# Kernel optimization log

Hardware: AMD Instinct MI355X
Metric: run time of the kernel (lower is better)

Reference implementation:

```python
import jax, jax.numpy as jnp
import numpy as np

INPUT_DIM = 512
OUTPUT_DIM = 512
NUM_BASIS = 16
GRID_MIN, GRID_MAX = -2.0, 2.0
LN_EPS = 1e-5


def rbf_basis(x):
    # x: [batch, input_dim] -> [batch, input_dim, num_basis]
    centers = jnp.linspace(GRID_MIN, GRID_MAX, NUM_BASIS, dtype=x.dtype)  # [K]
    h = (GRID_MAX - GRID_MIN) / (NUM_BASIS - 1)
    z = (x[..., None] - centers) / h
    return jnp.exp(-(z * z))


def setup_inputs() -> dict:
    key = jax.random.key(0)
    k1, k2, k3 = jax.random.split(key, 3)
    x = jax.random.normal(k1, (4096, INPUT_DIM), dtype=jnp.float32)
    weights = jax.random.normal(k2, (OUTPUT_DIM, INPUT_DIM, NUM_BASIS), dtype=jnp.float32) * 0.1
    base_weights = jax.random.normal(k3, (OUTPUT_DIM, INPUT_DIM), dtype=jnp.float32) * 0.1
    ln_gamma = jnp.ones((OUTPUT_DIM,), dtype=jnp.float32)
    ln_beta = jnp.zeros((OUTPUT_DIM,), dtype=jnp.float32)
    return {"x": x, "weights": weights, "base_weights": base_weights,
            "ln_gamma": ln_gamma, "ln_beta": ln_beta}


def reference(x, weights, base_weights, ln_gamma, ln_beta):
    # per-edge basis expansion: [B, I, K]
    basis = rbf_basis(x)
    # fused contraction replacing the nested python loops:
    # out[b, j] = sum_{i,k} basis[b, i, k] * weights[j, i, k]
    out = jnp.einsum('bik,jik->bj', basis, weights)
    # residual base activation path
    out = out + jax.nn.silu(x) @ base_weights.T
    # layer norm over output_dim
    mean = jnp.mean(out, axis=-1, keepdims=True)
    var = jnp.var(out, axis=-1, keepdims=True)
    out = (out - mean) * jax.lax.rsqrt(var + LN_EPS) * ln_gamma + ln_beta
    return out
```

## Files before the change

kernel.cpp:

```cpp
#include <hip/hip_runtime.h>
#include <hip/hip_bf16.h>


typedef __bf16 bf16x8 __attribute__((ext_vector_type(8)));
typedef __bf16 bf16x4 __attribute__((ext_vector_type(4)));
typedef float  f32x4  __attribute__((ext_vector_type(4)));

#define KT 8704
#define SPLITS 8
#define KS (KT / SPLITS)
#define NT2 (KS / 64)
#define CPE (4096 * 512)
#define ATILE (256 * 64)

__device__ __forceinline__ void gll16(const __bf16* g, __bf16* l) {
    __builtin_amdgcn_global_load_lds(
        (const __attribute__((address_space(1))) void*)g,
        (__attribute__((address_space(3))) void*)l, 16, 0, 0);
}

__global__ void prep_AB(const float* __restrict__ x, const float* __restrict__ W,
                        const float* __restrict__ Wb, __bf16* __restrict__ Asilu,
                        __bf16* __restrict__ B) {
    if (blockIdx.x < 1024) {
        int t = blockIdx.x * 256 + threadIdx.x;
        int e = t * 8;
        float4 v0 = *(const float4*)&x[e];
        float4 v1 = *(const float4*)&x[e + 4];
        float vs[8] = {v0.x, v0.y, v0.z, v0.w, v1.x, v1.y, v1.z, v1.w};
        bf16x8 o;
#pragma unroll
        for (int j = 0; j < 8; ++j) o[j] = (__bf16)(vs[j] / (1.0f + __expf(-vs[j])));
        *(bf16x8*)&Asilu[e] = o;
    } else {
        int t = (blockIdx.x - 1024) * 256 + threadIdx.x;
        int j = t / 2176;
        int c = (t - j * 2176) * 4;
        float4 v;
        if (c < 8192) v = *(const float4*)&W[(size_t)j * 8192 + c];
        else          v = *(const float4*)&Wb[(size_t)j * 512 + (c - 8192)];
        bf16x4 o;
        o[0] = (__bf16)v.x; o[1] = (__bf16)v.y; o[2] = (__bf16)v.z; o[3] = (__bf16)v.w;
        *(bf16x4*)&B[(size_t)j * KT + c] = o;
    }
}

__global__ __launch_bounds__(512, 2) void gemm_bt(const float* __restrict__ xg,
                                                  const __bf16* __restrict__ Sg,
                                                  const __bf16* __restrict__ B,
                                                  __bf16* __restrict__ Cp) {
    __shared__ __attribute__((aligned(16))) __bf16 As[2 * ATILE];
    __shared__ __attribute__((aligned(16))) __bf16 Bs[2 * ATILE];

    const int tid  = threadIdx.x;
    const int wave = tid >> 6, lane = tid & 63;
    const int q    = lane >> 4, r16 = lane & 15;
    const int m0 = blockIdx.x * 256, n0 = blockIdx.y * 256, k0 = blockIdx.z * KS;
    const int wm = wave >> 2, wn = wave & 3;

    const int sr = tid >> 3;
    const int sc = (tid & 7) ^ ((tid >> 4) & 7);
    const __bf16* gB0 = B + (size_t)(n0 + sr) * KT       + k0 + sc * 8;
    const __bf16* gB1 = B + (size_t)(n0 + 64  + sr) * KT + k0 + sc * 8;
    const __bf16* gB2 = B + (size_t)(n0 + 128 + sr) * KT + k0 + sc * 8;
    const __bf16* gB3 = B + (size_t)(n0 + 192 + sr) * KT + k0 + sc * 8;
    const __bf16* gS0 = Sg + (size_t)(m0 + sr) * 512       + sc * 8;
    const __bf16* gS1 = Sg + (size_t)(m0 + 64  + sr) * 512 + sc * 8;
    const __bf16* gS2 = Sg + (size_t)(m0 + 128 + sr) * 512 + sc * 8;
    const __bf16* gS3 = Sg + (size_t)(m0 + 192 + sr) * 512 + sc * 8;

    const int pr   = tid >> 1, pha = tid & 1;
    const int swzr = (pr >> 1) & 7;
    const int wb0  = pr * 64;
    const float* xrow = xg + (size_t)(m0 + pr) * 512 + 2 * pha;

    f32x4 acc[8][4] = {};

    const int swl = (r16 >> 1) & 7;
    const int qx0 = ((q)     ^ swl) * 8;
    const int qx1 = ((4 + q) ^ swl) * 8;
    const int aro = (wm * 128 + r16) * 64;
    const int bro = (wn * 64  + r16) * 64;

    auto write_basis = [&](float2 xv, int so) {
#pragma unroll
        for (int e = 0; e < 2; ++e) {
            const float xc = e ? xv.y : xv.x;
            const float zb = 3.75f * xc + 7.5f;
            const int   ci = 2 * pha + e;
            bf16x8 lo, hi;
#pragma unroll
            for (int j = 0; j < 8; ++j)  { float z = zb - (float)j;       lo[j]     = (__bf16)__expf(-z * z); }
#pragma unroll
            for (int j = 8; j < 16; ++j) { float z = zb - (float)j;       hi[j - 8] = (__bf16)__expf(-z * z); }
            *(bf16x8*)(As + so + wb0 + ((2 * ci)     ^ swzr) * 8) = lo;
            *(bf16x8*)(As + so + wb0 + ((2 * ci + 1) ^ swzr) * 8) = hi;
        }
    };

    float2 xv0 = *(const float2*)(xrow + (k0 >> 4));
    gll16(gB0, &Bs[(size_t)tid * 8]);
    gll16(gB1, &Bs[(size_t)(512 + tid) * 8]);
    gll16(gB2, &Bs[(size_t)(1024 + tid) * 8]);
    gll16(gB3, &Bs[(size_t)(1536 + tid) * 8]);
    write_basis(xv0, 0);
    __syncthreads();

    bf16x8 a[4], b[4];
    float2 xn = xv0;
    for (int u = 0; u < NT2; ++u) {
        const int s   = u & 1;
        const int cbo = s * ATILE;
        const int so1 = (s ^ 1) * ATILE;
        const int k1  = (u + 1) * 64;
        const int kn  = k0 + k1;
        const bool nb = kn < 8192;
        const int kk  = kn - 8192;

#pragma unroll
        for (int mi = 0; mi < 4; ++mi) a[mi] = *(const bf16x8*)(As + cbo + aro + mi * 1024 + qx0);
#pragma unroll
        for (int ni = 0; ni < 4; ++ni) b[ni] = *(const bf16x8*)(Bs + cbo + bro + ni * 1024 + qx0);
        gll16(gB0 + k1, &Bs[(size_t)(so1 + tid * 8)]);
        gll16(gB1 + k1, &Bs[(size_t)(so1 + (512 + tid) * 8)]);
        if (nb) xn = *(const float2*)(xrow + (kn >> 4));
        __builtin_amdgcn_s_setprio(1);
#pragma unroll
        for (int mi = 0; mi < 4; ++mi)
#pragma unroll
            for (int ni = 0; ni < 4; ++ni)
                acc[mi][ni] = __builtin_amdgcn_mfma_f32_16x16x32_bf16(a[mi], b[ni], acc[mi][ni], 0, 0, 0);
        __builtin_amdgcn_s_setprio(0);
        __builtin_amdgcn_s_barrier();

#pragma unroll
        for (int mi = 0; mi < 4; ++mi) a[mi] = *(const bf16x8*)(As + cbo + aro + (4 + mi) * 1024 + qx0);
        gll16(gB2 + k1, &Bs[(size_t)(so1 + (1024 + tid) * 8)]);
        gll16(gB3 + k1, &Bs[(size_t)(so1 + (1536 + tid) * 8)]);
        if (!nb) {
            gll16(gS0 + kk, &As[(size_t)(so1 + tid * 8)]);
            gll16(gS1 + kk, &As[(size_t)(so1 + (512 + tid) * 8)]);
        }
        __builtin_amdgcn_s_setprio(1);
#pragma unroll
        for (int mi = 0; mi < 4; ++mi)
#pragma unroll
            for (int ni = 0; ni < 4; ++ni)
                acc[4 + mi][ni] = __builtin_amdgcn_mfma_f32_16x16x32_bf16(a[mi], b[ni], acc[4 + mi][ni], 0, 0, 0);
        __builtin_amdgcn_s_setprio(0);
        __builtin_amdgcn_s_barrier();

#pragma unroll
        for (int mi = 0; mi < 4; ++mi) a[mi] = *(const bf16x8*)(As + cbo + aro + mi * 1024 + qx1);
#pragma unroll
        for (int ni = 0; ni < 4; ++ni) b[ni] = *(const bf16x8*)(Bs + cbo + bro + ni * 1024 + qx1);
        if (!nb) {
            gll16(gS2 + kk, &As[(size_t)(so1 + (1024 + tid) * 8)]);
            gll16(gS3 + kk, &As[(size_t)(so1 + (1536 + tid) * 8)]);
        }
        __builtin_amdgcn_s_setprio(1);
#pragma unroll
        for (int mi = 0; mi < 4; ++mi)
#pragma unroll
            for (int ni = 0; ni < 4; ++ni)
                acc[mi][ni] = __builtin_amdgcn_mfma_f32_16x16x32_bf16(a[mi], b[ni], acc[mi][ni], 0, 0, 0);
        __builtin_amdgcn_s_setprio(0);
        __builtin_amdgcn_s_barrier();

#pragma unroll
        for (int mi = 0; mi < 4; ++mi) a[mi] = *(const bf16x8*)(As + cbo + aro + (4 + mi) * 1024 + qx1);
        if (nb) write_basis(xn, so1);
        __builtin_amdgcn_s_setprio(1);
#pragma unroll
        for (int mi = 0; mi < 4; ++mi)
#pragma unroll
            for (int ni = 0; ni < 4; ++ni)
                acc[4 + mi][ni] = __builtin_amdgcn_mfma_f32_16x16x32_bf16(a[mi], b[ni], acc[4 + mi][ni], 0, 0, 0);
        __builtin_amdgcn_s_setprio(0);
        __syncthreads();
    }

    __bf16* Cb = Cp + (size_t)blockIdx.z * CPE;
#pragma unroll
    for (int mi = 0; mi < 8; ++mi) {
        const int row = m0 + wm * 128 + mi * 16 + q * 4;
#pragma unroll
        for (int ni = 0; ni < 4; ++ni) {
            const int col = n0 + wn * 64 + ni * 16 + r16;
#pragma unroll
            for (int r = 0; r < 4; ++r)
                Cb[(size_t)(row + r) * 512 + col] = (__bf16)acc[mi][ni][r];
        }
    }
}

__global__ void ln_kernel(const __bf16* __restrict__ Cp, const float* __restrict__ gamma,
                          const float* __restrict__ beta, float* __restrict__ out) {
    const int tid  = threadIdx.x;
    const int wave = tid >> 6, lane = tid & 63;
    const int row  = blockIdx.x * 4 + wave;
    const size_t base = (size_t)row * 512 + lane * 8;

    float v[8] = {};
    float s = 0.f, s2 = 0.f;
#pragma unroll
    for (int z = 0; z < SPLITS; ++z) {
        bf16x8 p = *(const bf16x8*)(Cp + (size_t)z * CPE + base);
#pragma unroll
        for (int j = 0; j < 8; ++j) v[j] += (float)p[j];
    }
#pragma unroll
    for (int j = 0; j < 8; ++j) { s += v[j]; s2 += v[j] * v[j]; }
#pragma unroll
    for (int m = 32; m >= 1; m >>= 1) {
        s  += __shfl_xor(s, m);
        s2 += __shfl_xor(s2, m);
    }
    const float mean = s * (1.0f / 512.0f);
    const float var  = s2 * (1.0f / 512.0f) - mean * mean;
    const float rs   = rsqrtf(var + 1e-5f);
    float4 o0, o1;
    const float4 g0 = *(const float4*)&gamma[lane * 8];
    const float4 g1 = *(const float4*)&gamma[lane * 8 + 4];
    const float4 b0 = *(const float4*)&beta[lane * 8];
    const float4 b1 = *(const float4*)&beta[lane * 8 + 4];
    o0.x = (v[0] - mean) * rs * g0.x + b0.x;
    o0.y = (v[1] - mean) * rs * g0.y + b0.y;
    o0.z = (v[2] - mean) * rs * g0.z + b0.z;
    o0.w = (v[3] - mean) * rs * g0.w + b0.w;
    o1.x = (v[4] - mean) * rs * g1.x + b1.x;
    o1.y = (v[5] - mean) * rs * g1.y + b1.y;
    o1.z = (v[6] - mean) * rs * g1.z + b1.z;
    o1.w = (v[7] - mean) * rs * g1.w + b1.w;
    *(float4*)&out[base]     = o0;
    *(float4*)&out[base + 4] = o1;
}

extern "C" void kernel_launch(void* const* d_in, const int* in_sizes, int n_in,
                              void* d_out, int out_size, void* d_ws, size_t ws_size,
                              hipStream_t stream) {
    const float* x     = (const float*)d_in[0];
    const float* W     = (const float*)d_in[1];
    const float* Wb    = (const float*)d_in[2];
    const float* gamma = (const float*)d_in[3];
    const float* beta  = (const float*)d_in[4];
    float* out = (float*)d_out;

    char* ws = (char*)d_ws;
    __bf16* Asilu = (__bf16*)ws;
    __bf16* Bm    = (__bf16*)(ws + 4194304);
    __bf16* Cp    = (__bf16*)(ws + 13107200);

    prep_AB<<<1024 + 4352, 256, 0, stream>>>(x, W, Wb, Asilu, Bm);
    dim3 g(16, 2, SPLITS);
    gemm_bt<<<g, 512, 0, stream>>>(x, Asilu, Bm, Cp);
    ln_kernel<<<1024, 256, 0, stream>>>(Cp, gamma, beta, out);
}
```

Baseline: 133.5 us.

## Pad A tile in LDS and split basis generation across two phases

The A tile in shared memory switches from an XOR-swizzled 64-wide layout to a padded 72-element row stride, which simplifies the address math for both reads and basis writes. Basis generation for the next tile is split into two halves spread over two MFMA phases instead of one burst. The silu tail tiles are now loaded into registers with ordinary global loads and stored to LDS, replacing direct global-to-LDS loads that could not target a padded layout. This raises LDS use and register pressure, and the register-staged loads may expose more latency.

```diff
diff --git a/kernel.cpp b/kernel.cpp
--- a/kernel.cpp
+++ b/kernel.cpp
@@ -11,7 +11,9 @@
 #define KS (KT / SPLITS)
 #define NT2 (KS / 64)
 #define CPE (4096 * 512)
-#define ATILE (256 * 64)
+#define AP 72
+#define ATILEA (256 * AP)
+#define ATILEB (256 * 64)
 
 __device__ __forceinline__ void gll16(const __bf16* g, __bf16* l) {
     __builtin_amdgcn_global_load_lds(
@@ -49,8 +51,8 @@
                                                   const __bf16* __restrict__ Sg,
                                                   const __bf16* __restrict__ B,
                                                   __bf16* __restrict__ Cp) {
-    __shared__ __attribute__((aligned(16))) __bf16 As[2 * ATILE];
-    __shared__ __attribute__((aligned(16))) __bf16 Bs[2 * ATILE];
+    __shared__ __attribute__((aligned(16))) __bf16 As[2 * ATILEA];
+    __shared__ __attribute__((aligned(16))) __bf16 Bs[2 * ATILEB];
 
     const int tid  = threadIdx.x;
     const int wave = tid >> 6, lane = tid & 63;
@@ -64,38 +66,35 @@
     const __bf16* gB1 = B + (size_t)(n0 + 64  + sr) * KT + k0 + sc * 8;
     const __bf16* gB2 = B + (size_t)(n0 + 128 + sr) * KT + k0 + sc * 8;
     const __bf16* gB3 = B + (size_t)(n0 + 192 + sr) * KT + k0 + sc * 8;
-    const __bf16* gS0 = Sg + (size_t)(m0 + sr) * 512       + sc * 8;
-    const __bf16* gS1 = Sg + (size_t)(m0 + 64  + sr) * 512 + sc * 8;
-    const __bf16* gS2 = Sg + (size_t)(m0 + 128 + sr) * 512 + sc * 8;
-    const __bf16* gS3 = Sg + (size_t)(m0 + 192 + sr) * 512 + sc * 8;
-
-    const int pr   = tid >> 1, pha = tid & 1;
-    const int swzr = (pr >> 1) & 7;
-    const int wb0  = pr * 64;
+    const int scA = tid & 7;
+    const __bf16* gSa0 = Sg + (size_t)(m0 + sr) * 512       + scA * 8;
+    const __bf16* gSa1 = Sg + (size_t)(m0 + 64  + sr) * 512 + scA * 8;
+    const __bf16* gSa2 = Sg + (size_t)(m0 + 128 + sr) * 512 + scA * 8;
+    const __bf16* gSa3 = Sg + (size_t)(m0 + 192 + sr) * 512 + scA * 8;
+
+    const int pr  = tid >> 1, pha = tid & 1;
+    const int wb0 = pr * AP;
     const float* xrow = xg + (size_t)(m0 + pr) * 512 + 2 * pha;
 
     f32x4 acc[8][4] = {};
 
+    const int qx0 = q * 8;
+    const int qx1 = (4 + q) * 8;
+    const int aro = (wm * 128 + r16) * AP;
     const int swl = (r16 >> 1) & 7;
-    const int qx0 = ((q)     ^ swl) * 8;
-    const int qx1 = ((4 + q) ^ swl) * 8;
-    const int aro = (wm * 128 + r16) * 64;
-    const int bro = (wn * 64  + r16) * 64;
-
-    auto write_basis = [&](float2 xv, int so) {
-#pragma unroll
-        for (int e = 0; e < 2; ++e) {
-            const float xc = e ? xv.y : xv.x;
-            const float zb = 3.75f * xc + 7.5f;
-            const int   ci = 2 * pha + e;
-            bf16x8 lo, hi;
-#pragma unroll
-            for (int j = 0; j < 8; ++j)  { float z = zb - (float)j;       lo[j]     = (__bf16)__expf(-z * z); }
-#pragma unroll
-            for (int j = 8; j < 16; ++j) { float z = zb - (float)j;       hi[j - 8] = (__bf16)__expf(-z * z); }
-            *(bf16x8*)(As + so + wb0 + ((2 * ci)     ^ swzr) * 8) = lo;
-            *(bf16x8*)(As + so + wb0 + ((2 * ci + 1) ^ swzr) * 8) = hi;
-        }
+    const int bx0 = ((q)     ^ swl) * 8;
+    const int bx1 = ((4 + q) ^ swl) * 8;
+    const int bro = (wn * 64 + r16) * 64;
+
+    auto wb_col = [&](float xc, int ci, int so) {
+        const float zb = 3.75f * xc + 7.5f;
+        bf16x8 lo, hi;
+#pragma unroll
+        for (int j = 0; j < 8; ++j)  { float z = zb - (float)j;  lo[j]     = (__bf16)__expf(-z * z); }
+#pragma unroll
+        for (int j = 8; j < 16; ++j) { float z = zb - (float)j;  hi[j - 8] = (__bf16)__expf(-z * z); }
+        *(bf16x8*)(As + so + wb0 + (2 * ci)     * 8) = lo;
+        *(bf16x8*)(As + so + wb0 + (2 * ci + 1) * 8) = hi;
     };
 
     float2 xv0 = *(const float2*)(xrow + (k0 >> 4));
@@ -103,26 +102,30 @@
     gll16(gB1, &Bs[(size_t)(512 + tid) * 8]);
     gll16(gB2, &Bs[(size_t)(1024 + tid) * 8]);
     gll16(gB3, &Bs[(size_t)(1536 + tid) * 8]);
-    write_basis(xv0, 0);
+    wb_col(xv0.x, 2 * pha,     0);
+    wb_col(xv0.y, 2 * pha + 1, 0);
     __syncthreads();
 
     bf16x8 a[4], b[4];
+    bf16x8 sv0, sv1, sv2, sv3;
     float2 xn = xv0;
     for (int u = 0; u < NT2; ++u) {
-        const int s   = u & 1;
-        const int cbo = s * ATILE;
-        const int so1 = (s ^ 1) * ATILE;
-        const int k1  = (u + 1) * 64;
-        const int kn  = k0 + k1;
-        const bool nb = kn < 8192;
-        const int kk  = kn - 8192;
-
-#pragma unroll
-        for (int mi = 0; mi < 4; ++mi) a[mi] = *(const bf16x8*)(As + cbo + aro + mi * 1024 + qx0);
-#pragma unroll
-        for (int ni = 0; ni < 4; ++ni) b[ni] = *(const bf16x8*)(Bs + cbo + bro + ni * 1024 + qx0);
-        gll16(gB0 + k1, &Bs[(size_t)(so1 + tid * 8)]);
-        gll16(gB1 + k1, &Bs[(size_t)(so1 + (512 + tid) * 8)]);
+        const int s    = u & 1;
+        const int cboA = s * ATILEA;
+        const int cboB = s * ATILEB;
+        const int so1A = (s ^ 1) * ATILEA;
+        const int so1B = (s ^ 1) * ATILEB;
+        const int k1   = (u + 1) * 64;
+        const int kn   = k0 + k1;
+        const bool nb  = kn < 8192;
+        const int kk   = kn - 8192;
+
+#pragma unroll
+        for (int mi = 0; mi < 4; ++mi) a[mi] = *(const bf16x8*)(As + cboA + aro + mi * 16 * AP + qx0);
+#pragma unroll
+        for (int ni = 0; ni < 4; ++ni) b[ni] = *(const bf16x8*)(Bs + cboB + bro + ni * 1024 + bx0);
+        gll16(gB0 + k1, &Bs[(size_t)(so1B + tid * 8)]);
+        gll16(gB1 + k1, &Bs[(size_t)(so1B + (512 + tid) * 8)]);
         if (nb) xn = *(const float2*)(xrow + (kn >> 4));
         __builtin_amdgcn_s_setprio(1);
 #pragma unroll
@@ -134,42 +137,49 @@
         __builtin_amdgcn_s_barrier();
 
 #pragma unroll
-        for (int mi = 0; mi < 4; ++mi) a[mi] = *(const bf16x8*)(As + cbo + aro + (4 + mi) * 1024 + qx0);
-        gll16(gB2 + k1, &Bs[(size_t)(so1 + (1024 + tid) * 8)]);
-        gll16(gB3 + k1, &Bs[(size_t)(so1 + (1536 + tid) * 8)]);
-        if (!nb) {
-            gll16(gS0 + kk, &As[(size_t)(so1 + tid * 8)]);
-            gll16(gS1 + kk, &As[(size_t)(so1 + (512 + tid) * 8)]);
+        for (int mi = 0; mi < 4; ++mi) a[mi] = *(const bf16x8*)(As + cboA + aro + (4 + mi) * 16 * AP + qx0);
+        gll16(gB2 + k1, &Bs[(size_t)(so1B + (1024 + tid) * 8)]);
+        gll16(gB3 + k1, &Bs[(size_t)(so1B + (1536 + tid) * 8)]);
+        __builtin_amdgcn_s_setprio(1);
+#pragma unroll
+        for (int mi = 0; mi < 4; ++mi)
+#pragma unroll
+            for (int ni = 0; ni < 4; ++ni)
+                acc[4 + mi][ni] = __builtin_amdgcn_mfma_f32_16x16x32_bf16(a[mi], b[ni], acc[4 + mi][ni], 0, 0, 0);
+        __builtin_amdgcn_s_setprio(0);
+        __builtin_amdgcn_s_barrier();
+
+#pragma unroll
+        for (int mi = 0; mi < 4; ++mi) a[mi] = *(const bf16x8*)(As + cboA + aro + mi * 16 * AP + qx1);
+#pragma unroll
+        for (int ni = 0; ni < 4; ++ni) b[ni] = *(const bf16x8*)(Bs + cboB + bro + ni * 1024 + bx1);
+        if (nb) {
+            wb_col(xn.x, 2 * pha, so1A);
+        } else {
+            sv0 = *(const bf16x8*)(gSa0 + kk);
+            sv1 = *(const bf16x8*)(gSa1 + kk);
+            sv2 = *(const bf16x8*)(gSa2 + kk);
+            sv3 = *(const bf16x8*)(gSa3 + kk);
         }
         __builtin_amdgcn_s_setprio(1);
 #pragma unroll
         for (int mi = 0; mi < 4; ++mi)
 #pragma unroll
             for (int ni = 0; ni < 4; ++ni)
-                acc[4 + mi][ni] = __builtin_amdgcn_mfma_f32_16x16x32_bf16(a[mi], b[ni], acc[4 + mi][ni], 0, 0, 0);
+                acc[mi][ni] = __builtin_amdgcn_mfma_f32_16x16x32_bf16(a[mi], b[ni], acc[mi][ni], 0, 0, 0);
         __builtin_amdgcn_s_setprio(0);
         __builtin_amdgcn_s_barrier();
 
 #pragma unroll
-        for (int mi = 0; mi < 4; ++mi) a[mi] = *(const bf16x8*)(As + cbo + aro + mi * 1024 + qx1);
-#pragma unroll
-        for (int ni = 0; ni < 4; ++ni) b[ni] = *(const bf16x8*)(Bs + cbo + bro + ni * 1024 + qx1);
-        if (!nb) {
-            gll16(gS2 + kk, &As[(size_t)(so1 + (1024 + tid) * 8)]);
-            gll16(gS3 + kk, &As[(size_t)(so1 + (1536 + tid) * 8)]);
+        for (int mi = 0; mi < 4; ++mi) a[mi] = *(const bf16x8*)(As + cboA + aro + (4 + mi) * 16 * AP + qx1);
+        if (nb) {
+            wb_col(xn.y, 2 * pha + 1, so1A);
+        } else {
+            *(bf16x8*)(As + so1A + (sr)       * AP + scA * 8) = sv0;
+            *(bf16x8*)(As + so1A + (sr + 64)  * AP + scA * 8) = sv1;
+            *(bf16x8*)(As + so1A + (sr + 128) * AP + scA * 8) = sv2;
+            *(bf16x8*)(As + so1A + (sr + 192) * AP + scA * 8) = sv3;
         }
-        __builtin_amdgcn_s_setprio(1);
-#pragma unroll
-        for (int mi = 0; mi < 4; ++mi)
-#pragma unroll
-            for (int ni = 0; ni < 4; ++ni)
-                acc[mi][ni] = __builtin_amdgcn_mfma_f32_16x16x32_bf16(a[mi], b[ni], acc[mi][ni], 0, 0, 0);
-        __builtin_amdgcn_s_setprio(0);
-        __builtin_amdgcn_s_barrier();
-
-#pragma unroll
-        for (int mi = 0; mi < 4; ++mi) a[mi] = *(const bf16x8*)(As + cbo + aro + (4 + mi) * 1024 + qx1);
-        if (nb) write_basis(xn, so1);
         __builtin_amdgcn_s_setprio(1);
 #pragma unroll
         for (int mi = 0; mi < 4; ++mi)
```

After: 133.9 us. Within noise of the previous version (+0.3%).
